# Performance work log

Measured on AMD Instinct MI355X. Metric: run time of the kernel, lower is better.

The kernel has to match this reference:

```python
import jax, jax.numpy as jnp
import numpy as np

P = 0.8  # DropConnect keep probability
KERNELS = (3, 2)


def eps_contract(core, x, ks):
    """Contract one EPS core with all sliding ks x ks windows of x.
    core: (out, q**(ks*ks)); x: (b, h, w, q) -> (b, h-ks+1, w-ks+1, out).
    Builds the window tensor-product incrementally (small fixed ks*ks loop)."""
    b, h, w, q = x.shape
    H, W = h - ks + 1, w - ks + 1
    prod = None
    for di in range(ks):
        for dj in range(ks):
            pix = x[:, di:di + H, dj:dj + W, :]  # (b, H, W, q)
            if prod is None:
                prod = pix
            else:
                prod = (prod[..., :, None] * pix[..., None, :]).reshape(b, H, W, -1)
    # prod: (b, H, W, q**(ks*ks))
    return jnp.einsum('bhwk,ok->bhwo', prod, core)


def dropconnect_epses(epses):
    """Bernoulli(P) mask each core's components, rescale by 1/P (training mode)."""
    mkey = jax.random.key(42)
    out = []
    for i, core in enumerate(epses):
        mask = (jax.random.uniform(jax.random.fold_in(mkey, i), core.shape) < P).astype(core.dtype)
        out.append(mask * core / P)
    return out


def setup_inputs() -> dict:
    key = jax.random.key(0)
    k0, k1, k2, k3 = jax.random.split(key, 4)
    b = 128
    x = jax.random.uniform(k0, (b, 28, 28, 2), jnp.float32)  # quantum-encoded image
    d0 = 2 ** (3 * 3)   # 512 : first core input dim (q=2, ks=3)
    d1 = 6 ** (2 * 2)   # 1296: second core input dim (q=6, ks=2)
    eps0 = jax.random.normal(k1, (6, d0), jnp.float32) * d0 ** -0.5
    eps1 = jax.random.normal(k2, (10, d1), jnp.float32) * d1 ** -0.5
    in_features = 25 * 25 * 10  # (28 - (3+2) + 2)^2 * out_q
    W = jax.random.normal(k3, (10, in_features), jnp.float32) * (in_features ** -0.5 / 4.0)
    bias = jnp.zeros((10,), jnp.float32)
    return {"x": x, "eps0": eps0, "eps1": eps1, "W": W, "bias": bias}


def reference(x, eps0, eps1, W, bias):
    e0, e1 = dropconnect_epses((eps0, eps1))
    h = eps_contract(e0, x, KERNELS[0])   # (b, 26, 26, 6)
    h = eps_contract(e1, h, KERNELS[1])   # (b, 25, 25, 10)
    flat = h.reshape(h.shape[0], -1)      # b (h w q)
    return flat @ W.T + bias
```

## Files before the change

### kernel.cpp

```cpp
#include <hip/hip_runtime.h>
#include <hip/hip_bf16.h>
#include <stdint.h>

typedef __attribute__((ext_vector_type(8))) short short8;
typedef __attribute__((ext_vector_type(4))) float floatx4;
typedef __attribute__((ext_vector_type(4))) int intx4;

__device__ __forceinline__ void threefry2x32(uint32_t k0, uint32_t k1,
                                             uint32_t& x0, uint32_t& x1) {
  const uint32_t ks2 = k0 ^ k1 ^ 0x1BD11BDAu;
  uint32_t ks[3] = {k0, k1, ks2};
  const int rot[8] = {13, 15, 26, 6, 17, 29, 16, 24};
  x0 += ks[0];
  x1 += ks[1];
#pragma unroll
  for (int i = 0; i < 5; ++i) {
#pragma unroll
    for (int j = 0; j < 4; ++j) {
      const int r = rot[(i & 1) * 4 + j];
      x0 += x1;
      x1 = (x1 << r) | (x1 >> (32 - r));
      x1 ^= x0;
    }
    x0 += ks[(i + 1) % 3];
    x1 += ks[(i + 2) % 3] + (uint32_t)(i + 1);
  }
}

__device__ __forceinline__ float dropmask(int core, int e, float v) {
  uint32_t f0 = 0u, f1 = (uint32_t)core;
  threefry2x32(0u, 42u, f0, f1);
  uint32_t a = 0u, b = (uint32_t)e;
  threefry2x32(f0, f1, a, b);
  uint32_t bits = a ^ b;
  float u = __uint_as_float((bits >> 9) | 0x3F800000u) - 1.0f;
  float m = (u < 0.8f) ? 1.0f : 0.0f;
  return v * m / 0.8f;
}

__device__ __forceinline__ unsigned short f2bf(float f) {
  uint32_t u = __float_as_uint(f);
  uint32_t r = u + 0x7fffu + ((u >> 16) & 1u);
  return (unsigned short)(r >> 16);
}

union B2I { __hip_bfloat162 b; int i; };
__device__ __forceinline__ int pk_bf16(float lo, float hi) {
  B2I u;
  u.b = __float22bfloat162_rn(make_float2(lo, hi));
  return u.i;
}
union Frag { intx4 i; short8 s; };

__global__ void prep_kernel(const float* __restrict__ eps0,
                            const float* __restrict__ eps1,
                            unsigned short* __restrict__ bsw1,
                            unsigned short* __restrict__ bsw2) {
  int idx = blockIdx.x * 256 + threadIdx.x;
  if (idx < 8192) {
    int j = idx & 7, L = (idx >> 3) & 63, c = idx >> 9;
    int o = L & 15, q = L >> 4;
    int k = c * 32 + q * 8 + j;
    float v = 0.0f;
    if (o < 6) {
      int e = o * 512 + k;
      v = dropmask(0, e, eps0[e]);
    }
    bsw1[idx] = f2bf(v);
  } else {
    int t2 = idx - 8192;
    int j = t2 & 7, L = (t2 >> 3) & 63, c = t2 >> 9;
    int o = L & 15, q = L >> 4;
    int t = 45 * q + c;
    int m = t / 5, nk = 8 * (t % 5) + j;
    float v = 0.0f;
    if (o < 10 && nk < 36) {
      int e = o * 1296 + m * 36 + nk;
      v = dropmask(1, e, eps1[e]);
    }
    bsw2[t2] = f2bf(v);
  }
}

__device__ __forceinline__ float sel6(const float a[6], int k) {
  float r = a[0];
  r = (k == 1) ? a[1] : r;
  r = (k == 2) ? a[2] : r;
  r = (k == 3) ? a[3] : r;
  r = (k == 4) ? a[4] : r;
  r = (k == 5) ? a[5] : r;
  return r;
}

__global__ __launch_bounds__(512, 2) void fused_kernel(
    const float* __restrict__ x, const unsigned short* __restrict__ bsw1,
    const unsigned short* __restrict__ bsw2, const float* __restrict__ W,
    const float* __restrict__ bias, float* __restrict__ out) {
  __shared__ float h_lds[4056];
  __shared__ float flat_lds[6250];
  __shared__ float red[8][10];

  const int b = blockIdx.x;
  const int tid = threadIdx.x;
  const int lane = tid & 63;
  const int wv = tid >> 6;
  const int col = lane & 15, q = lane >> 4;

  intx4 bfr1[16];
  const intx4* bsrc1 = (const intx4*)bsw1;
#pragma unroll
  for (int c = 0; c < 16; ++c) bfr1[c] = bsrc1[c * 64 + lane];

  const float2* x2 = (const float2*)x + b * 784;
#pragma unroll 1
  for (int tile = wv; tile < 43; tile += 8) {
    const int p_raw = tile * 16 + col;
    const int p = p_raw < 676 ? p_raw : 675;
    const int ii = p / 26, jj = p - (p / 26) * 26;

    float xv[9][2];
#pragma unroll
    for (int di = 0; di < 3; ++di)
#pragma unroll
      for (int dj = 0; dj < 3; ++dj) {
        float2 v = x2[(ii + di) * 28 + (jj + dj)];
        xv[di * 3 + dj][0] = v.x;
        xv[di * 3 + dj][1] = v.y;
      }

    float w3[8];
#pragma unroll
    for (int j = 0; j < 8; ++j)
      w3[j] = xv[6][(j >> 2) & 1] * xv[7][(j >> 1) & 1] * xv[8][j & 1];

    const float wq = xv[4][(q >> 1) & 1] * xv[5][q & 1];
    float t01[4], t23[4];
#pragma unroll
    for (int a = 0; a < 2; ++a)
#pragma unroll
      for (int d = 0; d < 2; ++d) {
        t01[a * 2 + d] = xv[0][a] * xv[1][d];
        t23[a * 2 + d] = xv[2][a] * xv[3][d] * wq;
      }

    floatx4 acc0 = {0.f, 0.f, 0.f, 0.f};
    floatx4 acc1 = {0.f, 0.f, 0.f, 0.f};
#pragma unroll
    for (int c = 0; c < 16; ++c) {
      Frag bf;
      bf.i = bfr1[c];
      const float w = t01[c >> 2] * t23[c & 3];
      Frag af;
      af.i.x = pk_bf16(w * w3[0], w * w3[1]);
      af.i.y = pk_bf16(w * w3[2], w * w3[3]);
      af.i.z = pk_bf16(w * w3[4], w * w3[5]);
      af.i.w = pk_bf16(w * w3[6], w * w3[7]);
      if (c & 1)
        acc1 = __builtin_amdgcn_mfma_f32_16x16x32_bf16(af.s, bf.s, acc1, 0, 0, 0);
      else
        acc0 = __builtin_amdgcn_mfma_f32_16x16x32_bf16(af.s, bf.s, acc0, 0, 0, 0);
    }
    const floatx4 acc = acc0 + acc1;
    if (col < 6) {
#pragma unroll
      for (int r = 0; r < 4; ++r) {
        const int pp = tile * 16 + q * 4 + r;
        if (pp < 676) h_lds[pp * 6 + col] = acc[r];
      }
    }
  }

  intx4 bfr2[45];
  const intx4* bsrc2 = (const intx4*)bsw2;
#pragma unroll
  for (int c = 0; c < 45; ++c) bfr2[c] = bsrc2[c * 64 + lane];

  __syncthreads();

#pragma unroll 1
  for (int tile = wv; tile < 40; tile += 8) {
    const int p_raw = tile * 16 + col;
    const int p = p_raw < 625 ? p_raw : 624;
    const int ii = p / 25, jj = p - (p / 25) * 25;
    const int hbase = (ii * 26 + jj) * 6;

    float h00[6], h01[6], h10[6], h11[6];
#pragma unroll
    for (int t = 0; t < 6; ++t) {
      h00[t] = h_lds[hbase + t];
      h01[t] = h_lds[hbase + 6 + t];
      h10[t] = h_lds[hbase + 156 + t];
      h11[t] = h_lds[hbase + 162 + t];
    }

    floatx4 acc0 = {0.f, 0.f, 0.f, 0.f};
    floatx4 acc1 = {0.f, 0.f, 0.f, 0.f};
#pragma unroll
    for (int d = 0; d < 9; ++d) {
      const int m = 9 * q + d;
      const int ia = (m * 43) >> 8;
      const int ic = m - ia * 6;
      const float p01 = sel6(h00, ia) * sel6(h01, ic);
      float ph[6];
#pragma unroll
      for (int a = 0; a < 6; ++a) ph[a] = p01 * h10[a];
#pragma unroll
      for (int e = 0; e < 5; ++e) {
        Frag bf;
        bf.i = bfr2[d * 5 + e];
        const int n0 = 8 * e;
        float av[8];
#pragma unroll
        for (int j = 0; j < 8; ++j) {
          const int n = n0 + j;
          av[j] = (n < 36) ? ph[n / 6] * h11[n % 6] : 0.0f;
        }
        Frag af;
        af.i.x = pk_bf16(av[0], av[1]);
        af.i.y = pk_bf16(av[2], av[3]);
        af.i.z = pk_bf16(av[4], av[5]);
        af.i.w = pk_bf16(av[6], av[7]);
        if (e & 1)
          acc1 = __builtin_amdgcn_mfma_f32_16x16x32_bf16(af.s, bf.s, acc1, 0, 0, 0);
        else
          acc0 = __builtin_amdgcn_mfma_f32_16x16x32_bf16(af.s, bf.s, acc0, 0, 0, 0);
      }
    }
    const floatx4 acc = acc0 + acc1;
    if (col < 10) {
#pragma unroll
      for (int r = 0; r < 4; ++r) {
        const int pp = tile * 16 + q * 4 + r;
        if (pp < 625) flat_lds[pp * 10 + col] = acc[r];
      }
    }
  }
  __syncthreads();

  float acc[10];
#pragma unroll
  for (int o = 0; o < 10; ++o) acc[o] = 0.0f;
  for (int f = tid; f < 6250; f += 512) {
    const float v = flat_lds[f];
#pragma unroll
    for (int o = 0; o < 10; ++o) acc[o] += v * W[o * 6250 + f];
  }
#pragma unroll
  for (int o = 0; o < 10; ++o) {
#pragma unroll
    for (int s = 32; s > 0; s >>= 1) acc[o] += __shfl_xor(acc[o], s, 64);
  }
  if (lane == 0) {
#pragma unroll
    for (int o = 0; o < 10; ++o) red[wv][o] = acc[o];
  }
  __syncthreads();
  if (tid < 10) {
    float r = bias[tid];
#pragma unroll
    for (int ww = 0; ww < 8; ++ww) r += red[ww][tid];
    out[b * 10 + tid] = r;
  }
}

extern "C" void kernel_launch(void* const* d_in, const int* in_sizes, int n_in,
                              void* d_out, int out_size, void* d_ws,
                              size_t ws_size, hipStream_t stream) {
  const float* x = (const float*)d_in[0];
  const float* eps0 = (const float*)d_in[1];
  const float* eps1 = (const float*)d_in[2];
  const float* W = (const float*)d_in[3];
  const float* bias = (const float*)d_in[4];
  float* out = (float*)d_out;

  char* wsb = (char*)d_ws;
  unsigned short* bsw1 = (unsigned short*)wsb;
  unsigned short* bsw2 = (unsigned short*)(wsb + 16384);

  hipLaunchKernelGGL(prep_kernel, dim3(122), dim3(256), 0, stream, eps0, eps1,
                     bsw1, bsw2);
  hipLaunchKernelGGL(fused_kernel, dim3(128), dim3(512), 0, stream, x, bsw1,
                     bsw2, W, bias, out);
}
```

Measured before the change: 103.8 us.

## Split each image across four blocks by output row bands with atomic reduction

The fused kernel now launches four blocks per image instead of one. Each block computes a band of output rows, plus the one-row halo of the first-stage activation it needs, and does a partial linear layer over its slice of W. Partial results are combined with atomicAdd into an output that the prep kernel zeroes, and only the first band adds the bias. This gives 512 blocks instead of 128 to fill the many compute units, at the cost of recomputing the halo rows, atomic traffic, and a float summation order that is no longer deterministic.

```diff
diff --git a/kernel.cpp b/kernel.cpp
--- a/kernel.cpp
+++ b/kernel.cpp
@@ -55,8 +55,10 @@
 __global__ void prep_kernel(const float* __restrict__ eps0,
                             const float* __restrict__ eps1,
                             unsigned short* __restrict__ bsw1,
-                            unsigned short* __restrict__ bsw2) {
+                            unsigned short* __restrict__ bsw2,
+                            float* __restrict__ out) {
   int idx = blockIdx.x * 256 + threadIdx.x;
+  if (idx < 1280) out[idx] = 0.0f;
   if (idx < 8192) {
     int j = idx & 7, L = (idx >> 3) & 63, c = idx >> 9;
     int o = L & 15, q = L >> 4;
@@ -96,11 +98,17 @@
     const float* __restrict__ x, const unsigned short* __restrict__ bsw1,
     const unsigned short* __restrict__ bsw2, const float* __restrict__ W,
     const float* __restrict__ bias, float* __restrict__ out) {
-  __shared__ float h_lds[4056];
-  __shared__ float flat_lds[6250];
+  __shared__ float h_lds[8 * 26 * 6];
+  __shared__ float flat_lds[7 * 25 * 10];
   __shared__ float red[8][10];
 
-  const int b = blockIdx.x;
+  const int bq = blockIdx.x;
+  const int b = bq >> 2;
+  const int r = bq & 3;
+  const int s0 = (r == 0) ? 0 : (1 + 6 * r);
+  const int ns = (r == 0) ? 7 : 6;
+  const int nh = ns + 1;
+
   const int tid = threadIdx.x;
   const int lane = tid & 63;
   const int wv = tid >> 6;
@@ -111,19 +119,22 @@
 #pragma unroll
   for (int c = 0; c < 16; ++c) bfr1[c] = bsrc1[c * 64 + lane];
 
+  const int npix1 = nh * 26;
+  const int tiles1 = (npix1 + 15) >> 4;
   const float2* x2 = (const float2*)x + b * 784;
 #pragma unroll 1
-  for (int tile = wv; tile < 43; tile += 8) {
+  for (int tile = wv; tile < tiles1; tile += 8) {
     const int p_raw = tile * 16 + col;
-    const int p = p_raw < 676 ? p_raw : 675;
-    const int ii = p / 26, jj = p - (p / 26) * 26;
+    const int p = p_raw < npix1 ? p_raw : npix1 - 1;
+    const int il = p / 26, jj = p - il * 26;
+    const int gi = s0 + il;
 
     float xv[9][2];
 #pragma unroll
     for (int di = 0; di < 3; ++di)
 #pragma unroll
       for (int dj = 0; dj < 3; ++dj) {
-        float2 v = x2[(ii + di) * 28 + (jj + dj)];
+        float2 v = x2[(gi + di) * 28 + (jj + dj)];
         xv[di * 3 + dj][0] = v.x;
         xv[di * 3 + dj][1] = v.y;
       }
@@ -163,9 +174,9 @@
     const floatx4 acc = acc0 + acc1;
     if (col < 6) {
 #pragma unroll
-      for (int r = 0; r < 4; ++r) {
-        const int pp = tile * 16 + q * 4 + r;
-        if (pp < 676) h_lds[pp * 6 + col] = acc[r];
+      for (int rr = 0; rr < 4; ++rr) {
+        const int pp = tile * 16 + q * 4 + rr;
+        if (pp < npix1) h_lds[pp * 6 + col] = acc[rr];
       }
     }
   }
@@ -177,12 +188,14 @@
 
   __syncthreads();
 
+  const int npix2 = ns * 25;
+  const int tiles2 = (npix2 + 15) >> 4;
 #pragma unroll 1
-  for (int tile = wv; tile < 40; tile += 8) {
+  for (int tile = wv; tile < tiles2; tile += 8) {
     const int p_raw = tile * 16 + col;
-    const int p = p_raw < 625 ? p_raw : 624;
-    const int ii = p / 25, jj = p - (p / 25) * 25;
-    const int hbase = (ii * 26 + jj) * 6;
+    const int p = p_raw < npix2 ? p_raw : npix2 - 1;
+    const int il = p / 25, jj = p - il * 25;
+    const int hbase = (il * 26 + jj) * 6;
 
     float h00[6], h01[6], h10[6], h11[6];
 #pragma unroll
@@ -229,21 +242,23 @@
     const floatx4 acc = acc0 + acc1;
     if (col < 10) {
 #pragma unroll
-      for (int r = 0; r < 4; ++r) {
-        const int pp = tile * 16 + q * 4 + r;
-        if (pp < 625) flat_lds[pp * 10 + col] = acc[r];
+      for (int rr = 0; rr < 4; ++rr) {
+        const int pp = tile * 16 + q * 4 + rr;
+        if (pp < npix2) flat_lds[pp * 10 + col] = acc[rr];
       }
     }
   }
   __syncthreads();
 
+  const int nf = npix2 * 10;
+  const int fg0 = s0 * 250;
   float acc[10];
 #pragma unroll
   for (int o = 0; o < 10; ++o) acc[o] = 0.0f;
-  for (int f = tid; f < 6250; f += 512) {
+  for (int f = tid; f < nf; f += 512) {
     const float v = flat_lds[f];
 #pragma unroll
-    for (int o = 0; o < 10; ++o) acc[o] += v * W[o * 6250 + f];
+    for (int o = 0; o < 10; ++o) acc[o] += v * W[o * 6250 + fg0 + f];
   }
 #pragma unroll
   for (int o = 0; o < 10; ++o) {
@@ -256,10 +271,10 @@
   }
   __syncthreads();
   if (tid < 10) {
-    float r = bias[tid];
-#pragma unroll
-    for (int ww = 0; ww < 8; ++ww) r += red[ww][tid];
-    out[b * 10 + tid] = r;
+    float v = (r == 0) ? bias[tid] : 0.0f;
+#pragma unroll
+    for (int ww = 0; ww < 8; ++ww) v += red[ww][tid];
+    atomicAdd(&out[b * 10 + tid], v);
   }
 }
 
@@ -278,7 +293,7 @@
   unsigned short* bsw2 = (unsigned short*)(wsb + 16384);
 
   hipLaunchKernelGGL(prep_kernel, dim3(122), dim3(256), 0, stream, eps0, eps1,
-                     bsw1, bsw2);
-  hipLaunchKernelGGL(fused_kernel, dim3(128), dim3(512), 0, stream, x, bsw1,
+                     bsw1, bsw2, out);
+  hipLaunchKernelGGL(fused_kernel, dim3(512), dim3(512), 0, stream, x, bsw1,
                      bsw2, W, bias, out);
 }
```

Result: slower. 119.2 us (+14.9%).
